# Optimization experiments

Measured on AMD Instinct MI355X. Metric: run time of the kernel, lower is better.

Reference implementation:

```python
import jax, jax.numpy as jnp
import numpy as np

sg = jax.lax.stop_gradient
EPS = 1e-6


def _mlp(x, ws, bs):
    # Linear+ReLU for all but last layer, final Linear has no activation
    for w, b in zip(ws[:-1], bs[:-1]):
        x = jax.nn.relu(x @ w + b)
    return x @ ws[-1] + bs[-1]


def _rotate_to(src, tgt):
    # Rotation-trick straight-through: rotate src onto tgt; rotation and
    # scaling are constants w.r.t. gradients (stop_gradient), grads flow via src.
    ns = jnp.linalg.norm(src, axis=-1, keepdims=True)
    nt = jnp.linalg.norm(tgt, axis=-1, keepdims=True)
    u = sg(src / jnp.clip(ns, EPS))
    q = sg(tgt / jnp.clip(nt, EPS))
    w = u + q
    w = sg(w / jnp.clip(jnp.linalg.norm(w, axis=-1, keepdims=True), EPS))
    rot = src - 2.0 * jnp.sum(src * w, -1, keepdims=True) * w \
          + 2.0 * jnp.sum(src * u, -1, keepdims=True) * q
    return rot * sg(nt / jnp.clip(ns, EPS))


def _residual_vq(z, codebooks):
    # codebooks: (Q, K, D). Sequential residual quantization (Q=8, small loop OK).
    residual = z
    quantized_out = jnp.zeros_like(z)
    all_idx, all_loss = [], []
    for cb in codebooks:  # cb: (K, D)
        # squared L2 distances via expansion: ||r||^2 - 2 r.c + ||c||^2
        d = jnp.sum(residual * residual, -1, keepdims=True) \
            - 2.0 * residual @ cb.T + jnp.sum(cb * cb, -1)[None, :]
        idx = jnp.argmin(d, axis=-1)                 # (B,)
        q = cb[idx]                                  # (B, D) gather
        all_loss.append(jnp.mean((residual - sg(q)) ** 2))  # commitment loss
        q_st = _rotate_to(residual, q)               # rotation-trick STE
        quantized_out = quantized_out + q_st
        residual = residual - sg(q)
        all_idx.append(idx)
    indices = jnp.stack(all_idx, axis=-1)            # (B, Q)
    commit_loss = jnp.stack(all_loss)                # (Q,)
    return quantized_out, indices, commit_loss


def setup_inputs() -> dict:
    key = jax.random.key(0)
    ks = jax.random.split(key, 16)
    B, IN, H0, H1, D, Q, K = 8192, 2048, 1024, 512, 256, 8, 2048

    def lin(k, fi, fo):
        s = 1.0 / np.sqrt(fi)
        kw, kb = jax.random.split(k)
        return (jax.random.uniform(kw, (fi, fo), jnp.float32, -s, s),
                jax.random.uniform(kb, (fo,), jnp.float32, -s, s))

    e_w0, e_b0 = lin(ks[0], IN, H0)
    e_w1, e_b1 = lin(ks[1], H0, H1)
    e_w2, e_b2 = lin(ks[2], H1, D)
    d_w0, d_b0 = lin(ks[3], D, H1)
    d_w1, d_b1 = lin(ks[4], H1, H0)
    d_w2, d_b2 = lin(ks[5], H0, IN)
    codebooks = jax.random.normal(ks[6], (Q, K, D), jnp.float32)
    x = jax.random.normal(ks[7], (B, IN), jnp.float32)
    return {"x": x,
            "e_w0": e_w0, "e_b0": e_b0, "e_w1": e_w1, "e_b1": e_b1,
            "e_w2": e_w2, "e_b2": e_b2,
            "d_w0": d_w0, "d_b0": d_b0, "d_w1": d_w1, "d_b1": d_b1,
            "d_w2": d_w2, "d_b2": d_b2, "codebooks": codebooks}


def reference(x, e_w0, e_b0, e_w1, e_b1, e_w2, e_b2,
              d_w0, d_b0, d_w1, d_b1, d_w2, d_b2, codebooks):
    encoded = _mlp(x, [e_w0, e_w1, e_w2], [e_b0, e_b1, e_b2])
    quantized, indices, commit_loss = _residual_vq(encoded, codebooks)
    decoded = _mlp(quantized, [d_w0, d_w1, d_w2], [d_b0, d_b1, d_b2])
    return decoded, indices, commit_loss
```

## Files before the change

### kernel.cpp

```cpp
#include <hip/hip_runtime.h>
#include <stdint.h>

#define B_   8192
#define IN_  2048
#define H0_  1024
#define H1_  512
#define D_   256
#define Q_   8
#define K_   2048

typedef unsigned long long u64;
typedef unsigned short u16;
typedef __attribute__((ext_vector_type(8))) short bf16x8;
typedef __attribute__((ext_vector_type(4))) float f32x4;

__device__ __forceinline__ u16 f2bf(float x) {
    unsigned u = __float_as_uint(x);
    return (u16)((u + 0x7fffu + ((u >> 16) & 1u)) >> 16);
}
__device__ __forceinline__ float bf2f(u16 h) {
    return __uint_as_float((unsigned)h << 16);
}
__device__ __forceinline__ void gload_lds16(const void* g, void* l) {
    __builtin_amdgcn_global_load_lds(
        (const __attribute__((address_space(1))) void*)g,
        (__attribute__((address_space(3))) void*)l, 16, 0, 0);
}
__device__ __forceinline__ unsigned fkey(float f) {
    unsigned u = __float_as_uint(f);
    return (u & 0x80000000u) ? ~u : (u | 0x80000000u);
}

#define MFMA_BF16 __builtin_amdgcn_mfma_f32_16x16x32_bf16

__global__ __launch_bounds__(256)
void cbpack_kernel(const float* __restrict__ cb, u16* __restrict__ f0,
                   u16* __restrict__ f1, u16* __restrict__ f2)
{
    const int g    = blockIdx.x * 4 + (threadIdx.x >> 6);
    const int lane = threadIdx.x & 63;
    const int q = g >> 10, rem = g & 1023, cg = rem >> 3, k = rem & 7;
    const int col = cg * 16 + (lane & 15);
    const int d0  = k * 32 + (lane >> 4) * 8;
    const float* src = cb + ((size_t)q * K_ + col) * D_ + d0;
    float4 va = *(const float4*)src, vb = *(const float4*)(src + 4);
    float xs[8] = {va.x, va.y, va.z, va.w, vb.x, vb.y, vb.z, vb.w};
    u16 h[8], m[8], l8[8];
#pragma unroll
    for (int e = 0; e < 8; e++) {
        h[e] = f2bf(xs[e]);
        float r1 = xs[e] - bf2f(h[e]);
        m[e] = f2bf(r1);
        r1 -= bf2f(m[e]);
        l8[e] = f2bf(r1);
    }
    const size_t off = ((size_t)g * 64 + lane) * 8;
    *(ushort4*)(f0 + off)     = make_ushort4(h[0], h[1], h[2], h[3]);
    *(ushort4*)(f0 + off + 4) = make_ushort4(h[4], h[5], h[6], h[7]);
    *(ushort4*)(f1 + off)     = make_ushort4(m[0], m[1], m[2], m[3]);
    *(ushort4*)(f1 + off + 4) = make_ushort4(m[4], m[5], m[6], m[7]);
    *(ushort4*)(f2 + off)     = make_ushort4(l8[0], l8[1], l8[2], l8[3]);
    *(ushort4*)(f2 + off + 4) = make_ushort4(l8[4], l8[5], l8[6], l8[7]);
}

#define ROWS 32
__global__ __launch_bounds__(512)
void vq_fused(const float* __restrict__ z,
              const float* __restrict__ CB,
              const u16* __restrict__ cbF0, const u16* __restrict__ cbF1,
              const u16* __restrict__ cbF2,
              const float* __restrict__ cnorm,
              u16* __restrict__ qplane,
              float* __restrict__ out_idx,
              float* __restrict__ loss_acc)
{
    __shared__ float rs[ROWS * 256];
    __shared__ u16 pl0[ROWS * 256];
    __shared__ u16 pl1[ROWS * 256];
    __shared__ u16 pl2[ROWS * 256];
    __shared__ u64 wmin[ROWS][8];
    __shared__ u64 winner[ROWS];

    const int tid  = threadIdx.x;
    const int lane = tid & 63;
    const int wv   = tid >> 6;
    const int row0 = blockIdx.x * ROWS;

#pragma unroll
    for (int j = 0; j < 4; j++) {
        int g = tid + j * 512;
        ((float4*)rs)[g] = ((const float4*)(z + (size_t)row0 * D_))[g];
    }
    __syncthreads();

    auto splitPlanes = [&]() {
#pragma unroll
        for (int j = 0; j < 2; j++) {
            int c = tid + j * 512;
            int r = c >> 5, kc = c & 31;
            const float* src = rs + r * 256 + kc * 8;
            int phys = kc ^ (r & 7);
            u16 h[8], m[8], l[8];
#pragma unroll
            for (int e = 0; e < 8; e++) {
                float x = src[e];
                h[e] = f2bf(x);
                float r1 = x - bf2f(h[e]);
                m[e] = f2bf(r1);
                r1 -= bf2f(m[e]);
                l[e] = f2bf(r1);
            }
            int o = r * 256 + phys * 8;
            *(ushort4*)(pl0 + o)     = make_ushort4(h[0], h[1], h[2], h[3]);
            *(ushort4*)(pl0 + o + 4) = make_ushort4(h[4], h[5], h[6], h[7]);
            *(ushort4*)(pl1 + o)     = make_ushort4(m[0], m[1], m[2], m[3]);
            *(ushort4*)(pl1 + o + 4) = make_ushort4(m[4], m[5], m[6], m[7]);
            *(ushort4*)(pl2 + o)     = make_ushort4(l[0], l[1], l[2], l[3]);
            *(ushort4*)(pl2 + o + 4) = make_ushort4(l[4], l[5], l[6], l[7]);
        }
    };
    splitPlanes();
    __syncthreads();

    for (int q = 0; q < Q_; q++) {
        const float* cnq = cnorm + (size_t)q * K_;

        u64 best8[2][4];
#pragma unroll
        for (int mf = 0; mf < 2; mf++)
#pragma unroll
            for (int r = 0; r < 4; r++) best8[mf][r] = ~0ull;

#pragma unroll
        for (int half = 0; half < 2; half++) {
            const int colh = wv * 256 + half * 128;
            const int cg0  = colh >> 4;
            f32x4 acc[2][8];
#pragma unroll
            for (int mf = 0; mf < 2; mf++)
#pragma unroll
                for (int n = 0; n < 8; n++) acc[mf][n] = (f32x4){0.f, 0.f, 0.f, 0.f};

            for (int k = 0; k < 8; k++) {
                bf16x8 a0[2], a1[2], a2[2];
#pragma unroll
                for (int mf = 0; mf < 2; mf++) {
                    int r = (lane & 15) + mf * 16;
                    int phys = (k * 4 + (lane >> 4)) ^ (r & 7);
                    int o = r * 256 + phys * 8;
                    a0[mf] = *(const bf16x8*)(pl0 + o);
                    a1[mf] = *(const bf16x8*)(pl1 + o);
                    a2[mf] = *(const bf16x8*)(pl2 + o);
                }
#pragma unroll
                for (int n = 0; n < 8; n++) {
                    size_t fb = (((size_t)(q << 10) + (cg0 + n) * 8 + k) << 9)
                                + lane * 8;
                    bf16x8 b0 = *(const bf16x8*)(cbF0 + fb);
                    bf16x8 b1 = *(const bf16x8*)(cbF1 + fb);
                    bf16x8 b2 = *(const bf16x8*)(cbF2 + fb);
#pragma unroll
                    for (int mf = 0; mf < 2; mf++) {
                        acc[mf][n] = MFMA_BF16(a0[mf], b0, acc[mf][n], 0, 0, 0);
                        acc[mf][n] = MFMA_BF16(a1[mf], b0, acc[mf][n], 0, 0, 0);
                        acc[mf][n] = MFMA_BF16(a0[mf], b1, acc[mf][n], 0, 0, 0);
                        acc[mf][n] = MFMA_BF16(a1[mf], b1, acc[mf][n], 0, 0, 0);
                        acc[mf][n] = MFMA_BF16(a2[mf], b0, acc[mf][n], 0, 0, 0);
                        acc[mf][n] = MFMA_BF16(a0[mf], b2, acc[mf][n], 0, 0, 0);
                    }
                }
            }
#pragma unroll
            for (int n = 0; n < 8; n++) {
                int col = colh + n * 16 + (lane & 15);
                float cn = cnq[col];
#pragma unroll
                for (int mf = 0; mf < 2; mf++)
#pragma unroll
                    for (int r = 0; r < 4; r++) {
                        float d = cn - 2.0f * acc[mf][n][r];
                        u64 p = ((u64)fkey(d) << 32) | (unsigned)col;
                        if (p < best8[mf][r]) best8[mf][r] = p;
                    }
            }
        }

#pragma unroll
        for (int mf = 0; mf < 2; mf++)
#pragma unroll
            for (int r = 0; r < 4; r++) {
                u64 p = best8[mf][r];
#pragma unroll
                for (int msk = 1; msk <= 8; msk <<= 1) {
                    u64 o = __shfl_xor(p, msk, 64);
                    if (o < p) p = o;
                }
                if ((lane & 15) == 0)
                    wmin[mf * 16 + (lane >> 4) * 4 + r][wv] = p;
            }
        __syncthreads();
        if (tid < ROWS) {
            u64 m = wmin[tid][0];
#pragma unroll
            for (int w2 = 1; w2 < 8; w2++) { u64 o = wmin[tid][w2]; if (o < m) m = o; }
            winner[tid] = m;
            out_idx[(size_t)(row0 + tid) * Q_ + q] = (float)(unsigned)(m & 0xffffffffu);
        }
        __syncthreads();

        float lsum = 0.f;
#pragma unroll
        for (int j = 0; j < 4; j++) {
            int g = tid + j * 512;
            int r = g >> 6;
            unsigned idx = (unsigned)(winner[r] & 0xffffffffu);
            const float4 cv = *(const float4*)(CB + ((size_t)q * K_ + idx) * D_ + (g & 63) * 4);
            float4 rv = ((float4*)rs)[g];
            float dx = rv.x - cv.x, dy = rv.y - cv.y,
                  dz = rv.z - cv.z, dw = rv.w - cv.w;
            lsum += dx * dx + dy * dy + dz * dz + dw * dw;
            ((float4*)rs)[g] = make_float4(dx, dy, dz, dw);
        }
#pragma unroll
        for (int o = 32; o > 0; o >>= 1) lsum += __shfl_down(lsum, o, 64);
        if (lane == 0) atomicAdd(&loss_acc[q], lsum);
        __syncthreads();

        if (q < Q_ - 1) { splitPlanes(); __syncthreads(); }
    }

#pragma unroll
    for (int j = 0; j < 2; j++) {
        int c = tid + j * 512;
        int e0 = c * 8;
        const float* zp = z + (size_t)row0 * D_ + e0;
        float4 za = *(const float4*)zp, zb = *(const float4*)(zp + 4);
        float4 ra = *(const float4*)(rs + e0), rb = *(const float4*)(rs + e0 + 4);
        *(ushort4*)(qplane + (size_t)row0 * D_ + e0) =
            make_ushort4(f2bf(za.x - ra.x), f2bf(za.y - ra.y),
                         f2bf(za.z - ra.z), f2bf(za.w - ra.w));
        *(ushort4*)(qplane + (size_t)row0 * D_ + e0 + 4) =
            make_ushort4(f2bf(zb.x - rb.x), f2bf(zb.y - rb.y),
                         f2bf(zb.z - rb.z), f2bf(zb.w - rb.w));
    }
}

template<int NSA, int NSB, int RELU, int NSO, int WF32>
__global__ __launch_bounds__(512)
void gemm2(const u16* __restrict__ A0, const u16* __restrict__ A1,
           const u16* __restrict__ A2,
           const u16* __restrict__ B0, const u16* __restrict__ B1,
           const u16* __restrict__ B2,
           const float* __restrict__ bias,
           float* __restrict__ C,
           u16* __restrict__ C0, u16* __restrict__ C1, u16* __restrict__ C2,
           int N, int Kd)
{
    constexpr int HALF = NSA * 16384 + NSB * 8192;
    __shared__ __align__(16) char smem[2 * HALF];
    const int tid  = threadIdx.x;
    const int lane = tid & 63;
    const int wid  = tid >> 6;
    const int wr   = wid >> 1, wc = wid & 1;

    const int nwg  = gridDim.x;
    const int orig = blockIdx.x;
    const int xcd  = orig & 7;
    const int q8 = nwg >> 3, r8 = nwg & 7;
    const int wgid = (xcd < r8 ? xcd * (q8 + 1)
                               : r8 * (q8 + 1) + (xcd - r8) * q8) + (orig >> 3);
    const int gx = N >> 7;
    const int bx = wgid % gx;
    const int by = wgid / gx;
    const int row0 = by * 256;
    const int col0 = bx * 128;

    const u16* asrc[3][2];
    const u16* bsrc[3];
#pragma unroll
    for (int h = 0; h < 2; h++) {
        int ch = h * 512 + tid;
        int r  = ch >> 2;
        int kc = (ch & 3) ^ ((r >> 1) & 3);
        size_t off = (size_t)(row0 + r) * Kd + kc * 8;
        asrc[0][h] = A0 + off;
        if constexpr (NSA >= 3) { asrc[1][h] = A1 + off; asrc[2][h] = A2 + off; }
    }
    {
        int r  = tid >> 2;
        int kc = (tid & 3) ^ ((r >> 1) & 3);
        size_t off = (size_t)(col0 + r) * Kd + kc * 8;
        bsrc[0] = B0 + off;
        if constexpr (NSB >= 3) { bsrc[1] = B1 + off; bsrc[2] = B2 + off; }
    }

    auto stage = [&](int c) {
        char* base = smem + c * HALF;
#pragma unroll
        for (int s = 0; s < NSA; s++)
#pragma unroll
            for (int h = 0; h < 2; h++) {
                gload_lds16(asrc[s][h], base + s * 16384 + (h * 512 + tid) * 16);
                asrc[s][h] += 32;
            }
#pragma unroll
        for (int s = 0; s < NSB; s++) {
            gload_lds16(bsrc[s], base + NSA * 16384 + s * 8192 + tid * 16);
            bsrc[s] += 32;
        }
    };

    f32x4 acc[4][4];
#pragma unroll
    for (int m = 0; m < 4; m++)
#pragma unroll
        for (int n = 0; n < 4; n++) acc[m][n] = (f32x4){0.f, 0.f, 0.f, 0.f};

    const unsigned fro = (unsigned)((lane & 15) * 64
        + (((lane >> 4) ^ (((lane & 15) >> 1) & 3)) * 16));

    const int nt = Kd >> 5;
    int cur = 0;
    stage(0);
    __syncthreads();

    for (int t = 0; t < nt; t++) {
        if (t + 1 < nt) stage(cur ^ 1);
        const char* base = smem + cur * HALF;
        bf16x8 bfr[4][3];
#pragma unroll
        for (int n = 0; n < 4; n++)
#pragma unroll
            for (int s = 0; s < NSB; s++)
                bfr[n][s] = *(const bf16x8*)(base + NSA * 16384 + s * 8192
                                             + (wc * 64 + n * 16) * 64 + fro);
#pragma unroll
        for (int m = 0; m < 4; m++) {
            bf16x8 af[3];
#pragma unroll
            for (int s = 0; s < NSA; s++)
                af[s] = *(const bf16x8*)(base + s * 16384
                                         + (wr * 64 + m * 16) * 64 + fro);
#pragma unroll
            for (int n = 0; n < 4; n++) {
                acc[m][n] = MFMA_BF16(af[0], bfr[n][0], acc[m][n], 0, 0, 0);
                if constexpr (NSA >= 3 && NSB >= 3) {
                    acc[m][n] = MFMA_BF16(af[1], bfr[n][0], acc[m][n], 0, 0, 0);
                    acc[m][n] = MFMA_BF16(af[0], bfr[n][1], acc[m][n], 0, 0, 0);
                    acc[m][n] = MFMA_BF16(af[1], bfr[n][1], acc[m][n], 0, 0, 0);
                    acc[m][n] = MFMA_BF16(af[2], bfr[n][0], acc[m][n], 0, 0, 0);
                    acc[m][n] = MFMA_BF16(af[0], bfr[n][2], acc[m][n], 0, 0, 0);
                }
            }
        }
        __syncthreads();
        cur ^= 1;
    }

    const int rbase = row0 + wr * 64 + (lane >> 4) * 4;
    const int cbase = col0 + wc * 64 + (lane & 15);
    float bv[4];
#pragma unroll
    for (int n = 0; n < 4; n++) bv[n] = bias[cbase + n * 16];
#pragma unroll
    for (int m = 0; m < 4; m++)
#pragma unroll
        for (int n = 0; n < 4; n++)
#pragma unroll
            for (int r = 0; r < 4; r++) {
                float o = acc[m][n][r] + bv[n];
                if constexpr (RELU) o = fmaxf(o, 0.f);
                size_t off = (size_t)(rbase + m * 16 + r) * N + (cbase + n * 16);
                if constexpr (WF32) C[off] = o;
                if constexpr (NSO >= 1) {
                    u16 p0 = f2bf(o);
                    C0[off] = p0;
                    if constexpr (NSO >= 3) {
                        float r1 = o - bf2f(p0);
                        u16 p1 = f2bf(r1);
                        C1[off] = p1;
                        r1 -= bf2f(p1);
                        C2[off] = f2bf(r1);
                    }
                }
            }
}

template<int NSA, int NSB, int RELU, int NSO, int WF32>
__global__ __launch_bounds__(256)
void gemm_mfma(const u16* __restrict__ A0, const u16* __restrict__ A1,
               const u16* __restrict__ A2,
               const u16* __restrict__ B0, const u16* __restrict__ B1,
               const u16* __restrict__ B2,
               const float* __restrict__ bias,
               float* __restrict__ C,
               u16* __restrict__ C0, u16* __restrict__ C1, u16* __restrict__ C2,
               int M, int N, int Kd)
{
    constexpr int NP = NSA + NSB;
    __shared__ __align__(16) char smem[NP * 8192];
    const int tid  = threadIdx.x;
    const int lane = tid & 63;
    const int wid  = tid >> 6;
    const int wr   = wid >> 1, wc = wid & 1;
    const int row0 = blockIdx.y * 128;
    const int col0 = blockIdx.x * 128;

    const u16* asrc[3][2];
    const u16* bsrc[3][2];
#pragma unroll
    for (int h = 0; h < 2; h++) {
        int ch = h * 256 + tid;
        int r  = ch >> 2;
        int kc = (ch & 3) ^ ((r >> 1) & 3);
        size_t aoff = (size_t)(row0 + r) * Kd + kc * 8;
        size_t boff = (size_t)(col0 + r) * Kd + kc * 8;
        asrc[0][h] = A0 + aoff;
        if constexpr (NSA >= 3) { asrc[1][h] = A1 + aoff; asrc[2][h] = A2 + aoff; }
        bsrc[0][h] = B0 + boff;
        if constexpr (NSB >= 3) { bsrc[1][h] = B1 + boff; bsrc[2][h] = B2 + boff; }
    }

    f32x4 acc[4][4];
#pragma unroll
    for (int m = 0; m < 4; m++)
#pragma unroll
        for (int n = 0; n < 4; n++) acc[m][n] = (f32x4){0.f, 0.f, 0.f, 0.f};

    const unsigned fro = (unsigned)((lane & 15) * 64
        + (((lane >> 4) ^ (((lane & 15) >> 1) & 3)) * 16));

    for (int k0 = 0; k0 < Kd; k0 += 32) {
#pragma unroll
        for (int s = 0; s < NSA; s++)
#pragma unroll
            for (int h = 0; h < 2; h++) {
                gload_lds16(asrc[s][h], smem + s * 8192 + (h * 256 + tid) * 16);
                asrc[s][h] += 32;
            }
#pragma unroll
        for (int s = 0; s < NSB; s++)
#pragma unroll
            for (int h = 0; h < 2; h++) {
                gload_lds16(bsrc[s][h],
                            smem + (NSA + s) * 8192 + (h * 256 + tid) * 16);
                bsrc[s][h] += 32;
            }
        __syncthreads();

        bf16x8 bfr[4][3];
#pragma unroll
        for (int n = 0; n < 4; n++)
#pragma unroll
            for (int s = 0; s < NSB; s++)
                bfr[n][s] = *(const bf16x8*)(smem + (NSA + s) * 8192
                                             + (wc * 64 + n * 16) * 64 + fro);
#pragma unroll
        for (int m = 0; m < 4; m++) {
            bf16x8 af[3];
#pragma unroll
            for (int s = 0; s < NSA; s++)
                af[s] = *(const bf16x8*)(smem + s * 8192
                                         + (wr * 64 + m * 16) * 64 + fro);
#pragma unroll
            for (int n = 0; n < 4; n++) {
                acc[m][n] = MFMA_BF16(af[0], bfr[n][0], acc[m][n], 0, 0, 0);
                if constexpr (NSA >= 3 && NSB >= 3) {
                    acc[m][n] = MFMA_BF16(af[1], bfr[n][0], acc[m][n], 0, 0, 0);
                    acc[m][n] = MFMA_BF16(af[0], bfr[n][1], acc[m][n], 0, 0, 0);
                    acc[m][n] = MFMA_BF16(af[1], bfr[n][1], acc[m][n], 0, 0, 0);
                    acc[m][n] = MFMA_BF16(af[2], bfr[n][0], acc[m][n], 0, 0, 0);
                    acc[m][n] = MFMA_BF16(af[0], bfr[n][2], acc[m][n], 0, 0, 0);
                }
            }
        }
        __syncthreads();
    }

    const int rbase = row0 + wr * 64 + (lane >> 4) * 4;
    const int cbase = col0 + wc * 64 + (lane & 15);
    float bv[4];
#pragma unroll
    for (int n = 0; n < 4; n++) bv[n] = bias[cbase + n * 16];
#pragma unroll
    for (int m = 0; m < 4; m++)
#pragma unroll
        for (int n = 0; n < 4; n++)
#pragma unroll
            for (int r = 0; r < 4; r++) {
                float o = acc[m][n][r] + bv[n];
                if constexpr (RELU) o = fmaxf(o, 0.f);
                size_t off = (size_t)(rbase + m * 16 + r) * N + (cbase + n * 16);
                if constexpr (WF32) C[off] = o;
                if constexpr (NSO >= 1) {
                    u16 p0 = f2bf(o);
                    C0[off] = p0;
                    if constexpr (NSO >= 3) {
                        float r1 = o - bf2f(p0);
                        u16 p1 = f2bf(r1);
                        C1[off] = p1;
                        r1 -= bf2f(p1);
                        C2[off] = f2bf(r1);
                    }
                }
            }
}

template<int NS>
__global__ __launch_bounds__(256)
void wsplit_kernel(const float* __restrict__ W, u16* __restrict__ T0,
                   u16* __restrict__ T1, u16* __restrict__ T2, int Kd, int N)
{
    __shared__ float t[32][33];
    const int tx = threadIdx.x & 31, ty = threadIdx.x >> 5;
    const int n0 = blockIdx.x * 32, k0 = blockIdx.y * 32;
#pragma unroll
    for (int r = 0; r < 4; r++)
        t[ty + r * 8][tx] = W[(size_t)(k0 + ty + r * 8) * N + n0 + tx];
    __syncthreads();
#pragma unroll
    for (int r = 0; r < 4; r++) {
        int n = n0 + ty + r * 8, k = k0 + tx;
        float v = t[tx][ty + r * 8];
        u16 h = f2bf(v);
        T0[(size_t)n * Kd + k] = h;
        if constexpr (NS >= 2) {
            float rr = v - bf2f(h);
            u16 m = f2bf(rr);
            T1[(size_t)n * Kd + k] = m;
            if constexpr (NS >= 3) { rr -= bf2f(m); T2[(size_t)n * Kd + k] = f2bf(rr); }
        }
    }
}

__global__ __launch_bounds__(256)
void esplit3_kernel(const float* __restrict__ src, u16* __restrict__ s0,
                    u16* __restrict__ s1, u16* __restrict__ s2)
{
    size_t i = (size_t)blockIdx.x * 256 + threadIdx.x;
    float4 v = ((const float4*)src)[i];
    float x[4] = {v.x, v.y, v.z, v.w};
    u16 h[4], m[4], l[4];
#pragma unroll
    for (int e = 0; e < 4; e++) {
        h[e] = f2bf(x[e]);
        float r1 = x[e] - bf2f(h[e]);
        m[e] = f2bf(r1);
        r1 -= bf2f(m[e]);
        l[e] = f2bf(r1);
    }
    ((ushort4*)s0)[i] = make_ushort4(h[0], h[1], h[2], h[3]);
    ((ushort4*)s1)[i] = make_ushort4(m[0], m[1], m[2], m[3]);
    ((ushort4*)s2)[i] = make_ushort4(l[0], l[1], l[2], l[3]);
}

__global__ void cnorm_kernel(const float* __restrict__ cb, float* __restrict__ cn)
{
    const int lane = threadIdx.x & 63;
    const int w = threadIdx.x >> 6;
    const int row = blockIdx.x * 4 + w;
    const float4 v = *(const float4*)(&cb[(size_t)row * D_ + lane * 4]);
    float s = v.x * v.x + v.y * v.y + v.z * v.z + v.w * v.w;
#pragma unroll
    for (int o = 32; o > 0; o >>= 1) s += __shfl_down(s, o, 64);
    if (lane == 0) cn[row] = s;
}

__global__ void loss_write_kernel(const float* __restrict__ loss_acc,
                                  float* __restrict__ out_loss)
{
    int q = threadIdx.x;
    if (q < Q_) out_loss[q] = loss_acc[q] * (1.0f / ((float)B_ * (float)D_));
}

extern "C" void kernel_launch(void* const* d_in, const int* in_sizes, int n_in,
                              void* d_out, int out_size, void* d_ws, size_t ws_size,
                              hipStream_t stream)
{
    const float* x    = (const float*)d_in[0];
    const float* e_w0 = (const float*)d_in[1];
    const float* e_b0 = (const float*)d_in[2];
    const float* e_w1 = (const float*)d_in[3];
    const float* e_b1 = (const float*)d_in[4];
    const float* e_w2 = (const float*)d_in[5];
    const float* e_b2 = (const float*)d_in[6];
    const float* d_w0 = (const float*)d_in[7];
    const float* d_b0 = (const float*)d_in[8];
    const float* d_w1 = (const float*)d_in[9];
    const float* d_b1 = (const float*)d_in[10];
    const float* d_w2 = (const float*)d_in[11];
    const float* d_b2 = (const float*)d_in[12];
    const float* codebooks = (const float*)d_in[13];

    float* out = (float*)d_out;
    float* out_decoded = out;
    float* out_idx     = out + (size_t)B_ * IN_;
    float* out_loss    = out_idx + (size_t)B_ * Q_;

    char* w = (char*)d_ws;
    auto alloc = [&](size_t bytes) {
        char* r = w; w += (bytes + 255) & ~(size_t)255; return r;
    };
    u16* ew0t = (u16*)alloc((size_t)3 * IN_ * H0_ * 2);
    u16* ew1t = (u16*)alloc((size_t)3 * H0_ * H1_ * 2);
    u16* ew2t = (u16*)alloc((size_t)3 * H1_ * D_ * 2);
    u16* dw0t = (u16*)alloc((size_t)D_ * H1_ * 2);
    u16* dw1t = (u16*)alloc((size_t)H1_ * H0_ * 2);
    u16* dw2t = (u16*)alloc((size_t)H0_ * IN_ * 2);
    u16* cbF  = (u16*)alloc((size_t)3 * Q_ * K_ * D_ * 2);
    float* cnorm = (float*)alloc((size_t)Q_ * K_ * 4);
    float* loss  = (float*)alloc(64);
    float* zbuf  = (float*)alloc((size_t)B_ * D_ * 4);
    u16* qplane  = (u16*)alloc((size_t)B_ * D_ * 2);
    char* regX = alloc((size_t)3 * B_ * IN_ * 2);
    u16* xp0 = (u16*)regX;
    u16* xp1 = xp0 + (size_t)B_ * IN_;
    u16* xp2 = xp1 + (size_t)B_ * IN_;
    u16* h1p0 = (u16*)regX;
    u16* h1p1 = h1p0 + (size_t)B_ * H1_;
    u16* h1p2 = h1p1 + (size_t)B_ * H1_;
    u16* dh1p = h1p2 + (size_t)B_ * H1_;
    u16* dh0p = dh1p + (size_t)B_ * H1_;
    char* regH = alloc((size_t)3 * B_ * H0_ * 2);
    u16* h0p0 = (u16*)regH;
    u16* h0p1 = h0p0 + (size_t)B_ * H0_;
    u16* h0p2 = h0p1 + (size_t)B_ * H0_;

    const size_t ew0s = (size_t)IN_ * H0_, ew1s = (size_t)H0_ * H1_,
                 ew2s = (size_t)H1_ * D_, cbsz = (size_t)Q_ * K_ * D_;

    hipMemsetAsync(loss, 0, 64, stream);
    esplit3_kernel<<<(size_t)B_ * IN_ / 1024, 256, 0, stream>>>(x, xp0, xp1, xp2);
    cbpack_kernel<<<2048, 256, 0, stream>>>(
        codebooks, cbF, cbF + cbsz, cbF + 2 * cbsz);
    wsplit_kernel<3><<<dim3(H0_ / 32, IN_ / 32), 256, 0, stream>>>(
        e_w0, ew0t, ew0t + ew0s, ew0t + 2 * ew0s, IN_, H0_);
    wsplit_kernel<3><<<dim3(H1_ / 32, H0_ / 32), 256, 0, stream>>>(
        e_w1, ew1t, ew1t + ew1s, ew1t + 2 * ew1s, H0_, H1_);
    wsplit_kernel<3><<<dim3(D_ / 32, H1_ / 32), 256, 0, stream>>>(
        e_w2, ew2t, ew2t + ew2s, ew2t + 2 * ew2s, H1_, D_);
    wsplit_kernel<1><<<dim3(H1_ / 32, D_ / 32), 256, 0, stream>>>(
        d_w0, dw0t, nullptr, nullptr, D_, H1_);
    wsplit_kernel<1><<<dim3(H0_ / 32, H1_ / 32), 256, 0, stream>>>(
        d_w1, dw1t, nullptr, nullptr, H1_, H0_);
    wsplit_kernel<1><<<dim3(IN_ / 32, H0_ / 32), 256, 0, stream>>>(
        d_w2, dw2t, nullptr, nullptr, H0_, IN_);
    cnorm_kernel<<<(Q_ * K_) / 4, 256, 0, stream>>>(codebooks, cnorm);

    gemm2<3, 3, 1, 3, 0><<<(H0_ / 128) * (B_ / 256), 512, 0, stream>>>(
        xp0, xp1, xp2, ew0t, ew0t + ew0s, ew0t + 2 * ew0s, e_b0,
        nullptr, h0p0, h0p1, h0p2, H0_, IN_);
    gemm_mfma<3, 3, 1, 3, 0><<<dim3(H1_ / 128, B_ / 128), 256, 0, stream>>>(
        h0p0, h0p1, h0p2, ew1t, ew1t + ew1s, ew1t + 2 * ew1s, e_b1,
        nullptr, h1p0, h1p1, h1p2, B_, H1_, H0_);
    gemm_mfma<3, 3, 0, 0, 1><<<dim3(D_ / 128, B_ / 128), 256, 0, stream>>>(
        h1p0, h1p1, h1p2, ew2t, ew2t + ew2s, ew2t + 2 * ew2s, e_b2,
        zbuf, nullptr, nullptr, nullptr, B_, D_, H1_);

    vq_fused<<<B_ / ROWS, 512, 0, stream>>>(
        zbuf, codebooks, cbF, cbF + cbsz, cbF + 2 * cbsz, cnorm,
        qplane, out_idx, loss);
    loss_write_kernel<<<1, 64, 0, stream>>>(loss, out_loss);

    gemm_mfma<1, 1, 1, 1, 0><<<dim3(H1_ / 128, B_ / 128), 256, 0, stream>>>(
        qplane, nullptr, nullptr, dw0t, nullptr, nullptr, d_b0,
        nullptr, dh1p, nullptr, nullptr, B_, H1_, D_);
    gemm2<1, 1, 1, 1, 0><<<(H0_ / 128) * (B_ / 256), 512, 0, stream>>>(
        dh1p, nullptr, nullptr, dw1t, nullptr, nullptr, d_b1,
        nullptr, dh0p, nullptr, nullptr, H0_, H1_);
    gemm2<1, 1, 0, 0, 1><<<(IN_ / 128) * (B_ / 256), 512, 0, stream>>>(
        dh0p, nullptr, nullptr, dw2t, nullptr, nullptr, d_b2,
        out_decoded, nullptr, nullptr, nullptr, IN_, H0_);
}
```

Before: 1.029 ms.

## Split VQ distance tile into 2-column groups to cut accumulator registers

Restructures the codebook-distance MFMA loop so each half processes four groups of two 16-column blocks instead of eight blocks at once, shrinking the live accumulator set from 16 to 4 f32x4 registers. B fragments for both columns are loaded ahead of the MFMAs. This lowers VGPR pressure, which may allow higher occupancy or avoid spills. In exchange, the A-plane LDS reads are repeated four times more per half, adding LDS traffic.

```diff
diff --git a/kernel.cpp b/kernel.cpp
--- a/kernel.cpp
+++ b/kernel.cpp
@@ -134,54 +134,63 @@
 #pragma unroll
         for (int half = 0; half < 2; half++) {
             const int colh = wv * 256 + half * 128;
-            const int cg0  = colh >> 4;
-            f32x4 acc[2][8];
-#pragma unroll
-            for (int mf = 0; mf < 2; mf++)
-#pragma unroll
-                for (int n = 0; n < 8; n++) acc[mf][n] = (f32x4){0.f, 0.f, 0.f, 0.f};
-
-            for (int k = 0; k < 8; k++) {
-                bf16x8 a0[2], a1[2], a2[2];
-#pragma unroll
-                for (int mf = 0; mf < 2; mf++) {
-                    int r = (lane & 15) + mf * 16;
-                    int phys = (k * 4 + (lane >> 4)) ^ (r & 7);
-                    int o = r * 256 + phys * 8;
-                    a0[mf] = *(const bf16x8*)(pl0 + o);
-                    a1[mf] = *(const bf16x8*)(pl1 + o);
-                    a2[mf] = *(const bf16x8*)(pl2 + o);
-                }
-#pragma unroll
-                for (int n = 0; n < 8; n++) {
-                    size_t fb = (((size_t)(q << 10) + (cg0 + n) * 8 + k) << 9)
-                                + lane * 8;
-                    bf16x8 b0 = *(const bf16x8*)(cbF0 + fb);
-                    bf16x8 b1 = *(const bf16x8*)(cbF1 + fb);
-                    bf16x8 b2 = *(const bf16x8*)(cbF2 + fb);
+            const int cg0h = colh >> 4;
+#pragma unroll
+            for (int gg = 0; gg < 4; gg++) {
+                f32x4 acc[2][2];
+#pragma unroll
+                for (int mf = 0; mf < 2; mf++)
+#pragma unroll
+                    for (int n = 0; n < 2; n++)
+                        acc[mf][n] = (f32x4){0.f, 0.f, 0.f, 0.f};
+
+                for (int k = 0; k < 8; k++) {
+                    bf16x8 a0[2], a1[2], a2[2];
 #pragma unroll
                     for (int mf = 0; mf < 2; mf++) {
-                        acc[mf][n] = MFMA_BF16(a0[mf], b0, acc[mf][n], 0, 0, 0);
-                        acc[mf][n] = MFMA_BF16(a1[mf], b0, acc[mf][n], 0, 0, 0);
-                        acc[mf][n] = MFMA_BF16(a0[mf], b1, acc[mf][n], 0, 0, 0);
-                        acc[mf][n] = MFMA_BF16(a1[mf], b1, acc[mf][n], 0, 0, 0);
-                        acc[mf][n] = MFMA_BF16(a2[mf], b0, acc[mf][n], 0, 0, 0);
-                        acc[mf][n] = MFMA_BF16(a0[mf], b2, acc[mf][n], 0, 0, 0);
+                        int r = (lane & 15) + mf * 16;
+                        int phys = (k * 4 + (lane >> 4)) ^ (r & 7);
+                        int o = r * 256 + phys * 8;
+                        a0[mf] = *(const bf16x8*)(pl0 + o);
+                        a1[mf] = *(const bf16x8*)(pl1 + o);
+                        a2[mf] = *(const bf16x8*)(pl2 + o);
+                    }
+                    bf16x8 b0[2], b1[2], b2[2];
+#pragma unroll
+                    for (int n = 0; n < 2; n++) {
+                        size_t fb = (((size_t)(q << 10)
+                                      + (cg0h + gg * 2 + n) * 8 + k) << 9)
+                                    + lane * 8;
+                        b0[n] = *(const bf16x8*)(cbF0 + fb);
+                        b1[n] = *(const bf16x8*)(cbF1 + fb);
+                        b2[n] = *(const bf16x8*)(cbF2 + fb);
+                    }
+#pragma unroll
+                    for (int n = 0; n < 2; n++) {
+#pragma unroll
+                        for (int mf = 0; mf < 2; mf++) {
+                            acc[mf][n] = MFMA_BF16(a0[mf], b0[n], acc[mf][n], 0, 0, 0);
+                            acc[mf][n] = MFMA_BF16(a1[mf], b0[n], acc[mf][n], 0, 0, 0);
+                            acc[mf][n] = MFMA_BF16(a0[mf], b1[n], acc[mf][n], 0, 0, 0);
+                            acc[mf][n] = MFMA_BF16(a1[mf], b1[n], acc[mf][n], 0, 0, 0);
+                            acc[mf][n] = MFMA_BF16(a2[mf], b0[n], acc[mf][n], 0, 0, 0);
+                            acc[mf][n] = MFMA_BF16(a0[mf], b2[n], acc[mf][n], 0, 0, 0);
+                        }
                     }
                 }
-            }
-#pragma unroll
-            for (int n = 0; n < 8; n++) {
-                int col = colh + n * 16 + (lane & 15);
-                float cn = cnq[col];
-#pragma unroll
-                for (int mf = 0; mf < 2; mf++)
-#pragma unroll
-                    for (int r = 0; r < 4; r++) {
-                        float d = cn - 2.0f * acc[mf][n][r];
-                        u64 p = ((u64)fkey(d) << 32) | (unsigned)col;
-                        if (p < best8[mf][r]) best8[mf][r] = p;
-                    }
+#pragma unroll
+                for (int n = 0; n < 2; n++) {
+                    int col = colh + (gg * 2 + n) * 16 + (lane & 15);
+                    float cn = cnq[col];
+#pragma unroll
+                    for (int mf = 0; mf < 2; mf++)
+#pragma unroll
+                        for (int r = 0; r < 4; r++) {
+                            float d = cn - 2.0f * acc[mf][n][r];
+                            u64 p = ((u64)fkey(d) << 32) | (unsigned)col;
+                            if (p < best8[mf][r]) best8[mf][r] = p;
+                        }
+                }
             }
         }
 
```

After: 1.358 ms. 32.0% more time.
